# Kernel optimization log

Hardware: AMD Instinct MI355X
Metric: run time of the kernel (lower is better)

Reference implementation:

```python
import jax, jax.numpy as jnp
import numpy as np

N = 50000      # nodes
E = 800000     # edges (avg degree 16)
F = 80         # hidden_channels (forced by Linear(80, 1))
L = 4          # num_layers
NG = 1024      # graphs in batch
NFEAT = 9      # OGB atom feature columns
VOCAB = 119    # max atom feature vocab
EPS_BN = 1e-5
EPS_STD = 1e-5


def setup_inputs() -> dict:
    key = jax.random.key(0)
    ks = jax.random.split(key, 20)
    s = 0.05
    x = jax.random.randint(ks[0], (N, NFEAT), 0, 2)
    edge_index = jax.random.randint(ks[1], (2, E), 0, N)
    batch = jnp.sort(jax.random.randint(ks[2], (N,), 0, NG))
    # avg_deg['log'] from the degree histogram == mean over nodes of log(deg+1)
    deg = jax.ops.segment_sum(jnp.ones((E,), jnp.float32), edge_index[1], num_segments=N)
    avg_deg_log = jnp.array([jnp.mean(jnp.log(deg + 1.0))], jnp.float32)
    atom_emb = jax.random.normal(ks[3], (NFEAT, VOCAB, F), jnp.float32) * s
    pre_W = jax.random.normal(ks[4], (L, 2 * F, F), jnp.float32) * s
    pre_b = jax.random.normal(ks[5], (L, F), jnp.float32) * s
    post_W = jax.random.normal(ks[6], (L, 13 * F, F), jnp.float32) * s
    post_b = jax.random.normal(ks[7], (L, F), jnp.float32) * s
    lin_W = jax.random.normal(ks[8], (L, F, F), jnp.float32) * s
    lin_b = jax.random.normal(ks[9], (L, F), jnp.float32) * s
    bn_gamma = 1.0 + jax.random.normal(ks[10], (L, F), jnp.float32) * 0.1
    bn_beta = jax.random.normal(ks[11], (L, F), jnp.float32) * 0.1
    bn_mean = jax.random.normal(ks[12], (L, F), jnp.float32) * 0.1
    bn_var = 0.5 + jax.random.uniform(ks[13], (L, F), jnp.float32)
    mlp_W = jax.random.normal(ks[14], (F, 1), jnp.float32) * s
    mlp_b = jax.random.normal(ks[15], (1,), jnp.float32) * s
    return {
        'x': x, 'edge_index': edge_index, 'batch': batch,
        'avg_deg_log': avg_deg_log, 'atom_emb': atom_emb,
        'pre_W': pre_W, 'pre_b': pre_b, 'post_W': post_W, 'post_b': post_b,
        'lin_W': lin_W, 'lin_b': lin_b,
        'bn_gamma': bn_gamma, 'bn_beta': bn_beta, 'bn_mean': bn_mean, 'bn_var': bn_var,
        'mlp_W': mlp_W, 'mlp_b': mlp_b,
    }


def _forward(x, edge_index, batch, avg_deg_log, atom_emb, pre_W, pre_b,
             post_W, post_b, lin_W, lin_b, bn_gamma, bn_beta, bn_mean, bn_var,
             mlp_W, mlp_b):
    # AtomEncoder: sum of per-column embeddings
    h = jnp.sum(atom_emb[jnp.arange(NFEAT)[None, :], x], axis=1)  # [N, F]
    src, dst = edge_index[0], edge_index[1]
    deg = jax.ops.segment_sum(jnp.ones((E,), h.dtype), dst, num_segments=N)
    has_edge = (deg > 0)[:, None]
    degc = jnp.maximum(deg, 1.0)[:, None]          # clamp(min=1)
    logd = jnp.log(degc + 1.0)                     # [N, 1]
    avg = avg_deg_log[0]
    for i in range(L):
        x_h = h
        # message: pre_nn(cat([x_i, x_j]))
        m = jnp.concatenate([h[dst], h[src]], axis=-1) @ pre_W[i] + pre_b[i]  # [E, F]
        s1 = jax.ops.segment_sum(m, dst, num_segments=N)
        s2 = jax.ops.segment_sum(m * m, dst, num_segments=N)
        mean = s1 / degc
        var = s2 / degc - mean * mean
        std = jnp.sqrt(jax.nn.relu(var) + EPS_STD)
        mn = jnp.where(has_edge, jax.ops.segment_min(m, dst, num_segments=N), 0.0)
        mx = jnp.where(has_edge, jax.ops.segment_max(m, dst, num_segments=N), 0.0)
        agg = jnp.concatenate([mean, mn, mx, std], axis=-1)  # [N, 4F]
        sc = logd / avg
        out = jnp.concatenate([agg, agg * sc, agg / sc], axis=-1)  # [N, 12F]
        out = jnp.concatenate([h, out], axis=-1) @ post_W[i] + post_b[i]  # [N, F]
        out = out @ lin_W[i] + lin_b[i]
        out = (out - bn_mean[i]) * (bn_gamma[i] / jnp.sqrt(bn_var[i] + EPS_BN)) + bn_beta[i]
        h = x_h + jax.nn.relu(out)  # dropout is identity in eval
    counts = jnp.maximum(jax.ops.segment_sum(jnp.ones((N,), h.dtype), batch, num_segments=NG), 1.0)
    g = jax.ops.segment_sum(h, batch, num_segments=NG) / counts[:, None]  # global_mean_pool
    return g @ mlp_W + mlp_b  # [NG, 1]


def reference(x, edge_index, batch, avg_deg_log, atom_emb, pre_W, pre_b,
              post_W, post_b, lin_W, lin_b, bn_gamma, bn_beta, bn_mean, bn_var,
              mlp_W, mlp_b):
    return _forward(x, edge_index, batch, avg_deg_log, atom_emb, pre_W, pre_b,
                    post_W, post_b, lin_W, lin_b, bn_gamma, bn_beta, bn_mean, bn_var,
                    mlp_W, mlp_b)
```

## Files before the change

kernel.cpp:

```cpp
#include <hip/hip_runtime.h>
#include <hip/hip_bf16.h>

#define NN 50000
#define NE 800000
#define FD 80
#define NGR 1024
#define NF 9

#define BSH 6
#define NBUCK ((NN + 63) >> 6)
#define CSH 12
#define NCH ((NE + 4095) >> 12)
#define BCAP 2048

using bf16 = __hip_bfloat16;
typedef __attribute__((ext_vector_type(8))) short bf16x8;
typedef __attribute__((ext_vector_type(4))) float f32x4;

static __device__ __forceinline__ float b2f(bf16 v){ return __bfloat162float(v); }
static __device__ __forceinline__ bf16 f2b(float v){ return __float2bfloat16(v); }
static __device__ __forceinline__ float rdw(const void* p, int i, int fl){
  return fl ? ((const float*)p)[i] : b2f(((const bf16*)p)[i]);
}
static __device__ __forceinline__ unsigned pk(float a, float b){
  bf16 x = f2b(a), y = f2b(b);
  return (unsigned)*(unsigned short*)&x | ((unsigned)*(unsigned short*)&y << 16);
}
static __device__ __forceinline__ bf16x8 ldsld8(const short* p){
  union { bf16x8 v; uint2 u[2]; } r;
  r.u[0] = *(const uint2*)(p);
  r.u[1] = *(const uint2*)(p + 4);
  return r.v;
}
static __device__ __forceinline__ void ldsst16(short* p, uint4 v){
  *(uint2*)(p)     = make_uint2(v.x, v.y);
  *(uint2*)(p + 4) = make_uint2(v.z, v.w);
}

__global__ void k_zero(int* __restrict__ p, int n){
  int t = blockIdx.x*256 + threadIdx.x;
  if (t < n) p[t] = 0;
}

__global__ void k_probe(const void* __restrict__ emb, int* __restrict__ flag){
  int t = blockIdx.x*256 + threadIdx.x;
  float v = b2f(((const bf16*)emb)[t]);
  if (!(fabsf(v) < 1e4f)) atomicOr(flag, 1);
}

__global__ __launch_bounds__(256) void k_prep_all(
    const void* __restrict__ preW, const void* __restrict__ preb,
    const void* __restrict__ postW, const void* __restrict__ postb,
    const void* __restrict__ linW, const void* __restrict__ linb,
    const void* __restrict__ bng, const void* __restrict__ bnb,
    const void* __restrict__ bnm, const void* __restrict__ bnv,
    const int* __restrict__ flag,
    bf16* __restrict__ pwb, bf16* __restrict__ Btl, bf16* __restrict__ Bt1,
    float* __restrict__ bias1, float* __restrict__ bias2)
{
  int fl = flag[0];
  int b = blockIdx.x;
  if (b < 1300){
    int t = b*256 + threadIdx.x;
    pwb[t] = f2b(rdw(postW, t, fl));
  } else if (b < 1420){
    int t = (b - 1300)*256 + threadIdx.x;
    int j = t % 96, c = (t/96) % 80, i = t/(96*80);
    float v = 0.f;
    if (j < 80){
      float gs = rdw(bng, i*80 + c, fl) * rsqrtf(rdw(bnv, i*80 + c, fl) + 1e-5f);
      v = rdw(linW, i*6400 + j*80 + c, fl) * gs;
    }
    Btl[t] = f2b(v);
  } else if (b < 1660){
    int t = (b - 1420)*256 + threadIdx.x;
    int k = t % 96, c = (t/96) % 160, i = t/(96*160);
    float v = 0.f;
    if (k < 80)
      v = (c < 80) ? rdw(preW, (i*160 + k)*80 + c, fl)
                   : rdw(preW, (i*160 + 80 + k)*80 + (c - 80), fl);
    Bt1[t] = f2b(v);
    if (k == 0) bias1[i*160 + c] = (c < 80) ? rdw(preb, i*80 + c, fl) : 0.f;
  } else {
    int t = (b - 1660)*256 + threadIdx.x;
    if (t >= 4*80) return;
    int i = t / 80, f = t - i*80;
    float s = 0.f;
    for (int j = 0; j < 80; j++)
      s += rdw(postb, i*80 + j, fl) * rdw(linW, (i*80 + j)*80 + f, fl);
    s += rdw(linb, t, fl);
    float gs = rdw(bng, t, fl) * rsqrtf(rdw(bnv, t, fl) + 1e-5f);
    bias2[t] = (s - rdw(bnm, t, fl)) * gs + rdw(bnb, t, fl);
  }
}

__global__ void k_prep_Bt2(const float* __restrict__ Wf, bf16* __restrict__ Bt2){
  int t = blockIdx.x*256 + threadIdx.x;
  if (t >= 4*240*416) return;
  int k = t % 416;
  int c = (t/416) % 240;
  int i = t/(416*240);
  float v = 0.f;
  if (k < 400){
    int blk = c/80, f = c - blk*80;
    if (blk == 0) v = Wf[(i*1040 + k)*80 + f];
    else if (k >= 80){
      int row = (blk == 1 ? 400 : 720) + (k - 80);
      v = Wf[(i*1040 + row)*80 + f];
    }
  }
  Bt2[t] = f2b(v);
}

__global__ void k_atom(const int* __restrict__ x, const void* __restrict__ emb,
                       const int* __restrict__ flag, float* __restrict__ h){
  int fl = flag[0];
  int gid = blockIdx.x*256 + threadIdx.x;
  if (gid >= NN*10) return;
  int n = gid / 10, fb = gid - n*10;
  int f0 = fb*8;
  int xr[NF];
  #pragma unroll
  for (int c = 0; c < NF; c++) xr[c] = x[n*NF + c];
  float s[8] = {0.f,0.f,0.f,0.f,0.f,0.f,0.f,0.f};
  if (fl){
    #pragma unroll
    for (int c = 0; c < NF; c++){
      const float* ep = (const float*)emb + (c*119 + xr[c])*80 + f0;
      float4 a = *(const float4*)ep, b = *(const float4*)(ep + 4);
      s[0]+=a.x; s[1]+=a.y; s[2]+=a.z; s[3]+=a.w;
      s[4]+=b.x; s[5]+=b.y; s[6]+=b.z; s[7]+=b.w;
    }
  } else {
    #pragma unroll
    for (int c = 0; c < NF; c++){
      const bf16* ep = (const bf16*)emb + (c*119 + xr[c])*80 + f0;
      uint4 u = *(const uint4*)ep;
      s[0]+=__uint_as_float(u.x<<16); s[1]+=__uint_as_float(u.x&0xffff0000u);
      s[2]+=__uint_as_float(u.y<<16); s[3]+=__uint_as_float(u.y&0xffff0000u);
      s[4]+=__uint_as_float(u.z<<16); s[5]+=__uint_as_float(u.z&0xffff0000u);
      s[6]+=__uint_as_float(u.w<<16); s[7]+=__uint_as_float(u.w&0xffff0000u);
    }
  }
  float* hp = h + n*80 + f0;
  *(float4*)hp       = make_float4(s[0],s[1],s[2],s[3]);
  *(float4*)(hp + 4) = make_float4(s[4],s[5],s[6],s[7]);
}


__global__ __launch_bounds__(256) void k_hist(const int* __restrict__ ei,
                                              int* __restrict__ chunkcnt){
  __shared__ int hist[NBUCK];
  int c = blockIdx.x, t = threadIdx.x;
  for (int i = t; i < NBUCK; i += 256) hist[i] = 0;
  __syncthreads();
  #pragma unroll
  for (int j = 0; j < 16; j++){
    int e = (c << CSH) + j*256 + t;
    if (e < NE) atomicAdd(&hist[ei[NE + e] >> BSH], 1);
  }
  __syncthreads();
  for (int i = t; i < NBUCK; i += 256) chunkcnt[c*NBUCK + i] = hist[i];
}

__global__ __launch_bounds__(256) void k_cscan(int* __restrict__ chunkcnt,
                                               int* __restrict__ btotal){
  __shared__ int buf[256];
  int b = blockIdx.x, t = threadIdx.x;
  int v[4]; int s = 0;
  #pragma unroll
  for (int j = 0; j < 4; j++){
    int c = t*4 + j;
    v[j] = (c < NCH) ? chunkcnt[c*NBUCK + b] : 0;
    s += v[j];
  }
  buf[t] = s;
  __syncthreads();
  for (int off = 1; off < 256; off <<= 1){
    int xv = (t >= off) ? buf[t - off] : 0;
    __syncthreads();
    buf[t] += xv;
    __syncthreads();
  }
  int excl = buf[t] - s;
  #pragma unroll
  for (int j = 0; j < 4; j++){
    int c = t*4 + j;
    if (c < NCH){ chunkcnt[c*NBUCK + b] = excl; excl += v[j]; }
  }
  if (t == 255) btotal[b] = buf[255];
}

__global__ __launch_bounds__(256) void k_bscan(const int* __restrict__ btotal,
                                               int* __restrict__ bbase){
  __shared__ int buf[256];
  int t = threadIdx.x;
  int v[4]; int s = 0;
  #pragma unroll
  for (int j = 0; j < 4; j++){
    int c = t*4 + j;
    v[j] = (c < NBUCK) ? btotal[c] : 0;
    s += v[j];
  }
  buf[t] = s;
  __syncthreads();
  for (int off = 1; off < 256; off <<= 1){
    int xv = (t >= off) ? buf[t - off] : 0;
    __syncthreads();
    buf[t] += xv;
    __syncthreads();
  }
  int excl = buf[t] - s;
  #pragma unroll
  for (int j = 0; j < 4; j++){
    int c = t*4 + j;
    if (c < NBUCK){ bbase[c] = excl; excl += v[j]; }
  }
  if (t == 255) bbase[NBUCK] = buf[255];
}

__global__ __launch_bounds__(256) void k_place(const int* __restrict__ ei,
                        const int* __restrict__ chunkcnt, const int* __restrict__ bbase,
                        int* __restrict__ staging){
  __shared__ int basep[NBUCK];
  __shared__ int cur[NBUCK];
  int c = blockIdx.x, t = threadIdx.x;
  for (int i = t; i < NBUCK; i += 256){
    basep[i] = chunkcnt[c*NBUCK + i] + bbase[i];
    cur[i] = 0;
  }
  __syncthreads();
  #pragma unroll
  for (int j = 0; j < 16; j++){
    int e = (c << CSH) + j*256 + t;
    if (e < NE){
      int d = ei[NE + e], s = ei[e];
      int b = d >> BSH;
      int r = atomicAdd(&cur[b], 1);
      staging[basep[b] + r] = (s << BSH) | (d & 63);
    }
  }
}

__global__ __launch_bounds__(256) void k_csr(const int* __restrict__ staging,
                        const int* __restrict__ bbase, const void* __restrict__ avgp,
                        const int* __restrict__ flag, int* __restrict__ rowptr,
                        float* __restrict__ scf, float* __restrict__ invf,
                        int* __restrict__ colidx){
  __shared__ int lcnt[64], lrp[64], lcur[64];
  __shared__ int colbuf[BCAP];
  int b = blockIdx.x, t = threadIdx.x;
  int base = bbase[b];
  int cnt  = bbase[b+1] - base;
  if (t < 64){ lcnt[t] = 0; lcur[t] = 0; }
  __syncthreads();
  for (int i = t; i < cnt; i += 256)
    atomicAdd(&lcnt[staging[base + i] & 63], 1);
  __syncthreads();
  if (t < 64) lrp[t] = lcnt[t];
  __syncthreads();
  for (int off = 1; off < 64; off <<= 1){
    int xv = (t < 64 && t >= off) ? lrp[t - off] : 0;
    __syncthreads();
    if (t < 64) lrp[t] += xv;
    __syncthreads();
  }
  int n0 = b << BSH;
  if (t < 64){
    int ex = lrp[t] - lcnt[t];
    lrp[t] = ex;
    int n = n0 + t;
    if (n < NN){
      rowptr[n] = base + ex;
      float degc = (float)(lcnt[t] > 0 ? lcnt[t] : 1);
      float logd = logf(degc + 1.f);
      float avg = rdw(avgp, 0, flag[0]);
      scf[n] = logd / avg;
      invf[n] = avg / logd;
    }
  }
  if (b == 0 && t == 0) rowptr[NN] = NE;
  __syncthreads();
  if (cnt <= BCAP){
    for (int i = t; i < cnt; i += 256){
      int v = staging[base + i];
      int l = v & 63;
      int pos = lrp[l] + atomicAdd(&lcur[l], 1);
      colbuf[pos] = v >> BSH;
    }
    __syncthreads();
    for (int i = t; i < cnt; i += 256)
      colidx[base + i] = colbuf[i];
  } else {
    for (int i = t; i < cnt; i += 256){
      int v = staging[base + i];
      int l = v & 63;
      int pos = lrp[l] + atomicAdd(&lcur[l], 1);
      colidx[base + pos] = v >> BSH;
    }
  }
}

template<int AF32, int OUTMODE, int K_, int AST>
__global__ __launch_bounds__(256) void k_mgemm(
    const void* __restrict__ A1p, int s1, int KA,
    const bf16* __restrict__ A2, int s2, int KB,
    const bf16* __restrict__ Btp, int Bts, int Ncols,
    const float* __restrict__ bias,
    void* __restrict__ Cbase, void* __restrict__ Cp2, int Cstride, int M,
    int lA1b, int lBtb, int lCb)
{
  const void* A1 = (const char*)A1p + (size_t)blockIdx.z*lA1b;
  const bf16* Bt = (const bf16*)((const char*)Btp + (size_t)blockIdx.z*lBtb);
  void* Cp = (char*)Cbase + (size_t)blockIdx.z*lCb;

  constexpr int NKT = K_ / 32;
  __shared__ short As[64*AST];
  __shared__ short Bs[256*44];

  const int tid = threadIdx.x;
  const int row0 = blockIdx.x * 64;
  const int wave = tid >> 6, lane = tid & 63;
  const int wc = wave * 64;
  const int m16 = lane & 15, q = lane >> 4;

  const int ra = tid >> 2, ka = (tid & 3) * 8;
  const int cb = tid >> 2, kb = (tid & 3) * 8;

  f32x4 acc[4][4] = {};
  uint4 pb[4];

#define LOADB(k0_) { int kgb = (k0_) + kb;                                     \
    _Pragma("unroll")                                                          \
    for (int j = 0; j < 4; j++){                                               \
      int col = cb + j*64;                                                     \
      pb[j].x = pb[j].y = pb[j].z = pb[j].w = 0u;                              \
      if (col < Ncols) pb[j] = *(const uint4*)(Bt + col*Bts + kgb);            \
    } }

  LOADB(0);

  {
    const int grow = row0 + ra;
    uint4 tA[NKT];
    #pragma unroll
    for (int c = 0; c < NKT; c++){
      int kg = c*32 + ka;
      uint4 pa; pa.x = pa.y = pa.z = pa.w = 0u;
      if (grow < M){
        if (kg < KA){
          if (AF32){
            const float* ap = (const float*)A1 + grow*s1 + kg;
            float4 f0 = *(const float4*)ap;
            float4 f1 = *(const float4*)(ap + 4);
            pa.x = pk(f0.x, f0.y); pa.y = pk(f0.z, f0.w);
            pa.z = pk(f1.x, f1.y); pa.w = pk(f1.z, f1.w);
          } else {
            pa = *(const uint4*)((const bf16*)A1 + grow*s1 + kg);
          }
        } else if (kg - KA < KB){
          pa = *(const uint4*)(A2 + grow*s2 + (kg - KA));
        }
      }
      tA[c] = pa;
    }
    #pragma unroll
    for (int c = 0; c < NKT; c++)
      ldsst16(&As[ra*AST + c*32 + ka], tA[c]);
  }
  __syncthreads();

  #pragma unroll
  for (int ks = 0; ks < NKT; ks++){
    #pragma unroll
    for (int j = 0; j < 4; j++)
      ldsst16(&Bs[(cb + j*64)*44 + kb], pb[j]);
    __syncthreads();

    if (ks + 1 < NKT) LOADB((ks + 1)*32);

    bf16x8 af[4], bfv[4];
    #pragma unroll
    for (int rt = 0; rt < 4; rt++)
      af[rt] = ldsld8(&As[(rt*16 + m16)*AST + ks*32 + q*8]);
    #pragma unroll
    for (int ct = 0; ct < 4; ct++)
      bfv[ct] = ldsld8(&Bs[(wc + ct*16 + m16)*44 + q*8]);
    #pragma unroll
    for (int rt = 0; rt < 4; rt++)
      #pragma unroll
      for (int ct = 0; ct < 4; ct++)
        acc[rt][ct] = __builtin_amdgcn_mfma_f32_16x16x32_bf16(af[rt], bfv[ct], acc[rt][ct], 0, 0, 0);
    __syncthreads();
  }
#undef LOADB

  #pragma unroll
  for (int rt = 0; rt < 4; rt++){
    #pragma unroll
    for (int rr = 0; rr < 4; rr++){
      int row = row0 + rt*16 + q*4 + rr;
      if (row >= M) continue;
      #pragma unroll
      for (int ct = 0; ct < 4; ct++){
        int col = wc + ct*16 + m16;
        if (col >= Ncols) continue;
        float v = acc[rt][ct][rr] + (bias ? bias[col] : 0.f);
        if (OUTMODE == 1) ((float*)Cp)[row*Cstride + col] = v;
        else {
          if (col < 80) ((bf16*)Cp )[row*80 + col]      = f2b(v);
          else          ((bf16*)Cp2)[row*80 + col - 80] = f2b(v);
        }
      }
    }
  }
}

__global__ __launch_bounds__(256) void k_g2(
    const float* __restrict__ h, const bf16* __restrict__ agg,
    const bf16* __restrict__ Bt, const float* __restrict__ bias2v,
    const float* __restrict__ scf, const float* __restrict__ invf,
    float* __restrict__ hp,
    const bf16* __restrict__ Bt1n, const float* __restrict__ bias1n,
    bf16* __restrict__ Ua, bf16* __restrict__ Ub)
{
  constexpr int AST = 420, NKT = 13;
  __shared__ short As[32*AST];
  __shared__ short Bs[256*44];
  bf16* eL = (bf16*)As;
  bf16* hA = (bf16*)(As + 8192);

  const int tid = threadIdx.x;
  const int row0 = blockIdx.x * 32;
  const int wave = tid >> 6, lane = tid & 63;
  const int wc = wave * 64;
  const int m16 = lane & 15, q = lane >> 4;
  const int ra = tid >> 3;
  const int ka0 = (tid & 7) * 8;
  const int cb = tid >> 2, kb = (tid & 3) * 8;

  f32x4 acc[2][4] = {};
  uint4 pb[4];

#define LOADB2(k0_) { int kgb = (k0_) + kb;                                    \
    _Pragma("unroll")                                                          \
    for (int j = 0; j < 4; j++){                                               \
      int col = cb + j*64;                                                     \
      pb[j].x = pb[j].y = pb[j].z = pb[j].w = 0u;                              \
      if (col < 240) pb[j] = *(const uint4*)(Bt + col*416 + kgb);              \
    } }

  LOADB2(0);

  {
    const int grow = row0 + ra;
    uint4 tA[7];
    #pragma unroll
    for (int c = 0; c < 7; c++){
      int kg = ka0 + c*64;
      uint4 pa; pa.x = pa.y = pa.z = pa.w = 0u;
      if (kg < 416 && grow < NN){
        if (kg < 80){
          const float* ap = h + grow*80 + kg;
          float4 f0 = *(const float4*)ap;
          float4 f1 = *(const float4*)(ap + 4);
          pa.x = pk(f0.x, f0.y); pa.y = pk(f0.z, f0.w);
          pa.z = pk(f1.x, f1.y); pa.w = pk(f1.z, f1.w);
        } else if (kg < 400){
          pa = *(const uint4*)(agg + grow*320 + (kg - 80));
        }
      }
      tA[c] = pa;
    }
    #pragma unroll
    for (int c = 0; c < 7; c++){
      int kg = ka0 + c*64;
      if (kg < 416) ldsst16(&As[ra*AST + kg], tA[c]);
    }
  }
  __syncthreads();

  #pragma unroll
  for (int ks = 0; ks < NKT; ks++){
    #pragma unroll
    for (int j = 0; j < 4; j++)
      ldsst16(&Bs[(cb + j*64)*44 + kb], pb[j]);
    __syncthreads();

    if (ks + 1 < NKT) LOADB2((ks + 1)*32);

    bf16x8 af[2], bfv[4];
    #pragma unroll
    for (int rt = 0; rt < 2; rt++)
      af[rt] = ldsld8(&As[(rt*16 + m16)*AST + ks*32 + q*8]);
    #pragma unroll
    for (int ct = 0; ct < 4; ct++)
      bfv[ct] = ldsld8(&Bs[(wc + ct*16 + m16)*44 + q*8]);
    #pragma unroll
    for (int rt = 0; rt < 2; rt++)
      #pragma unroll
      for (int ct = 0; ct < 4; ct++)
        acc[rt][ct] = __builtin_amdgcn_mfma_f32_16x16x32_bf16(af[rt], bfv[ct], acc[rt][ct], 0, 0, 0);
    __syncthreads();
  }
#undef LOADB2

  uint4 pb1[4];
  if (Bt1n){
    #pragma unroll
    for (int j = 0; j < 4; j++){
      int col = cb + j*64;
      pb1[j].x = pb1[j].y = pb1[j].z = pb1[j].w = 0u;
      if (col < 160) pb1[j] = *(const uint4*)(Bt1n + col*96 + kb);
    }
  }

  #pragma unroll
  for (int rt = 0; rt < 2; rt++){
    #pragma unroll
    for (int ct = 0; ct < 4; ct++){
      int col = wc + ct*16 + m16;
      if (col >= 240) continue;
      #pragma unroll
      for (int rr = 0; rr < 4; rr++){
        int r = rt*16 + q*4 + rr;
        eL[r*248 + col] = f2b(acc[rt][ct][rr]);
      }
    }
  }
  __syncthreads();

  #pragma unroll
  for (int i = 0; i < 10; i++){
    int idx = tid + i*256;
    int r = idx / 80, c = idx - r*80;
    int row = row0 + r;
    if (row < NN){
      float P = b2f(eL[r*248 + c]);
      float Q = b2f(eL[r*248 + 80 + c]);
      float R = b2f(eL[r*248 + 160 + c]);
      float o = P + scf[row]*Q + invf[row]*R + bias2v[c];
      float hn = hp[row*80 + c] + fmaxf(o, 0.f);
      hp[row*80 + c] = hn;
      if (Bt1n) hA[r*100 + c] = f2b(hn);
    } else if (Bt1n && idx < 32*80){
      hA[r*100 + c] = f2b(0.f);
    }
  }
  if (Bt1n && tid < 128){
    int r = tid >> 2, off = 80 + (tid & 3)*4;
    *(uint2*)&hA[r*100 + off] = make_uint2(0u, 0u);
  }
  __syncthreads();

  if (Bt1n){
    f32x4 acc2[2][4] = {};
    #pragma unroll
    for (int ks = 0; ks < 3; ks++){
      #pragma unroll
      for (int j = 0; j < 4; j++)
        ldsst16(&Bs[(cb + j*64)*44 + kb], pb1[j]);
      __syncthreads();

      if (ks + 1 < 3){
        int kgb = (ks + 1)*32 + kb;
        #pragma unroll
        for (int j = 0; j < 4; j++){
          int col = cb + j*64;
          pb1[j].x = pb1[j].y = pb1[j].z = pb1[j].w = 0u;
          if (col < 160) pb1[j] = *(const uint4*)(Bt1n + col*96 + kgb);
        }
      }

      bf16x8 af[2], bfv[4];
      #pragma unroll
      for (int rt = 0; rt < 2; rt++)
        af[rt] = ldsld8((const short*)hA + (rt*16 + m16)*100 + ks*32 + q*8);
      #pragma unroll
      for (int ct = 0; ct < 4; ct++)
        bfv[ct] = ldsld8(&Bs[(wc + ct*16 + m16)*44 + q*8]);
      #pragma unroll
      for (int rt = 0; rt < 2; rt++)
        #pragma unroll
        for (int ct = 0; ct < 4; ct++)
          acc2[rt][ct] = __builtin_amdgcn_mfma_f32_16x16x32_bf16(af[rt], bfv[ct], acc2[rt][ct], 0, 0, 0);
      __syncthreads();
    }
    #pragma unroll
    for (int rt = 0; rt < 2; rt++){
      #pragma unroll
      for (int rr = 0; rr < 4; rr++){
        int row = row0 + rt*16 + q*4 + rr;
        if (row >= NN) continue;
        #pragma unroll
        for (int ct = 0; ct < 4; ct++){
          int col = wc + ct*16 + m16;
          if (col >= 160) continue;
          float v = acc2[rt][ct][rr] + bias1n[col];
          if (col < 80) Ua[row*80 + col]      = f2b(v);
          else          Ub[row*80 + col - 80] = f2b(v);
        }
      }
    }
  }
}

__global__ __launch_bounds__(256) void k_agg(const bf16* __restrict__ Ua,
                      const bf16* __restrict__ Ub,
                      const int* __restrict__ rowptr,
                      const int* __restrict__ colidx, bf16* __restrict__ agg)
{
  int lane = threadIdx.x & 63;
  int slot = lane / 20;
  int n = blockIdx.x*12 + (threadIdx.x >> 6)*3 + slot;
  if (slot >= 3 || n >= NN) return;
  int fo = (lane - slot*20) * 4;
  int rs = rowptr[n], re = rowptr[n+1];
  int deg = re - rs;

  float a[4];
  {
    uint2 ua = *(const uint2*)(Ua + n*80 + fo);
    a[0] = __uint_as_float(ua.x << 16);
    a[1] = __uint_as_float(ua.x & 0xffff0000u);
    a[2] = __uint_as_float(ua.y << 16);
    a[3] = __uint_as_float(ua.y & 0xffff0000u);
  }
  float sb[4] = {0.f,0.f,0.f,0.f}, sq[4] = {0.f,0.f,0.f,0.f};
  float mn[4] = {1e30f,1e30f,1e30f,1e30f}, mx[4] = {-1e30f,-1e30f,-1e30f,-1e30f};

#define ACC2(w, o) { \
    float b0 = __uint_as_float((w) << 16); \
    float b1 = __uint_as_float((w) & 0xffff0000u); \
    sb[o] += b0; sq[o] += b0*b0; mn[o] = fminf(mn[o],b0); mx[o] = fmaxf(mx[o],b0); \
    sb[o+1] += b1; sq[o+1] += b1*b1; mn[o+1] = fminf(mn[o+1],b1); mx[o+1] = fmaxf(mx[o+1],b1); }

  for (int e = rs; e < re; e += 8){
    int cnt = re - e; if (cnt > 8) cnt = 8;
    int s[8];
    #pragma unroll
    for (int j = 0; j < 8; j++) s[j] = (j < cnt) ? colidx[e + j] : s[0];
    uint2 u[8];
    #pragma unroll
    for (int j = 0; j < 8; j++) u[j] = *(const uint2*)(Ub + s[j]*80 + fo);
    #pragma unroll
    for (int j = 0; j < 8; j++){
      if (j < cnt){ ACC2(u[j].x, 0); ACC2(u[j].y, 2); }
    }
  }
#undef ACC2

  float degc = (float)(deg > 0 ? deg : 1);
  float inv = 1.f/degc;
  float dm = (float)deg;
  float mean0, mean1, v0, v1, sd0, sd1, lo0, lo1, hi0, hi1;

  mean0 = (dm*a[0] + sb[0])*inv; mean1 = (dm*a[1] + sb[1])*inv;
  v0 = (dm*a[0]*a[0] + 2.f*a[0]*sb[0] + sq[0])*inv - mean0*mean0;
  v1 = (dm*a[1]*a[1] + 2.f*a[1]*sb[1] + sq[1])*inv - mean1*mean1;
  sd0 = sqrtf(fmaxf(v0,0.f)+1e-5f); sd1 = sqrtf(fmaxf(v1,0.f)+1e-5f);
  lo0 = deg>0 ? a[0]+mn[0] : 0.f; lo1 = deg>0 ? a[1]+mn[1] : 0.f;
  hi0 = deg>0 ? a[0]+mx[0] : 0.f; hi1 = deg>0 ? a[1]+mx[1] : 0.f;
  unsigned o0 = pk(mean0, mean1);
  unsigned l0 = pk(lo0, lo1), h0 = pk(hi0, hi1), t0 = pk(sd0, sd1);

  mean0 = (dm*a[2] + sb[2])*inv; mean1 = (dm*a[3] + sb[3])*inv;
  v0 = (dm*a[2]*a[2] + 2.f*a[2]*sb[2] + sq[2])*inv - mean0*mean0;
  v1 = (dm*a[3]*a[3] + 2.f*a[3]*sb[3] + sq[3])*inv - mean1*mean1;
  sd0 = sqrtf(fmaxf(v0,0.f)+1e-5f); sd1 = sqrtf(fmaxf(v1,0.f)+1e-5f);
  lo0 = deg>0 ? a[2]+mn[2] : 0.f; lo1 = deg>0 ? a[3]+mn[3] : 0.f;
  hi0 = deg>0 ? a[2]+mx[2] : 0.f; hi1 = deg>0 ? a[3]+mx[3] : 0.f;
  unsigned o1 = pk(mean0, mean1);
  unsigned l1 = pk(lo0, lo1), h1 = pk(hi0, hi1), t1 = pk(sd0, sd1);

  bf16* ag = agg + n*320 + fo;
  *(uint2*)(ag)       = make_uint2(o0, o1);
  *(uint2*)(ag + 80)  = make_uint2(l0, l1);
  *(uint2*)(ag + 160) = make_uint2(h0, h1);
  *(uint2*)(ag + 240) = make_uint2(t0, t1);
}

__global__ __launch_bounds__(128) void k_poolmlp(const float* __restrict__ h,
                        const int* __restrict__ batch,
                        const void* __restrict__ mlpW, const void* __restrict__ mlpb,
                        const int* __restrict__ flag, void* __restrict__ outp){
  __shared__ float sred[128];
  __shared__ int sb[2];
  int g = blockIdx.x;
  int t = threadIdx.x;
  if (t < 2){
    int target = g + t;
    int lo = 0, hi = NN;
    while (lo < hi){ int mid = (lo + hi) >> 1; if (batch[mid] < target) lo = mid + 1; else hi = mid; }
    sb[t] = lo;
  }
  __syncthreads();
  int lo = sb[0], hi = sb[1];
  float s = 0.f;
  if (t < 80)
    for (int n = lo; n < hi; n++) s += h[n*80 + t];
  int fl = flag[0];
  float wv = (t < 80) ? rdw(mlpW, t, fl) : 0.f;
  sred[t] = s * wv;
  __syncthreads();
  for (int off = 64; off > 0; off >>= 1){
    if (t < off) sred[t] += sred[t + off];
    __syncthreads();
  }
  if (t == 0){
    float cnt = (float)(hi - lo); if (cnt < 1.f) cnt = 1.f;
    float r = sred[0]/cnt + rdw(mlpb, 0, fl);
    if (fl) ((float*)outp)[g] = r;
    else    ((bf16*)outp)[g] = f2b(r);
  }
}

extern "C" void kernel_launch(void* const* d_in, const int* in_sizes, int n_in,
                              void* d_out, int out_size, void* d_ws, size_t ws_size,
                              hipStream_t stream)
{
  const int*  x     = (const int*) d_in[0];
  const int*  ei    = (const int*) d_in[1];
  const int*  batch = (const int*) d_in[2];
  const void* avgp  = d_in[3];
  const void* aemb  = d_in[4];
  const void* preW  = d_in[5];
  const void* preb  = d_in[6];
  const void* postW = d_in[7];
  const void* postb = d_in[8];
  const void* linW  = d_in[9];
  const void* linb  = d_in[10];
  const void* bng   = d_in[11];
  const void* bnb   = d_in[12];
  const void* bnm   = d_in[13];
  const void* bnv   = d_in[14];
  const void* mlpW  = d_in[15];
  const void* mlpb  = d_in[16];

  char* w = (char*)d_ws;
  int*   flag   = (int*)  (w + 400000);
  int*   rowptr = (int*)  (w + 401280);
  int*   colidx = (int*)  (w + 601344);
  float* scf    = (float*)(w + 3801344);
  float* invf   = (float*)(w + 4001344);
  float* bias1  = (float*)(w + 4201344);
  float* bias2  = (float*)(w + 4203904);
  bf16*  Btl    = (bf16*) (w + 4205184);
  bf16*  Bt1    = (bf16*) (w + 4266624);
  bf16*  Bt2    = (bf16*) (w + 4389504);
  float* h      = (float*)(w + 5188224);
  bf16*  Ua     = (bf16*) (w + 21188224);
  bf16*  Ub     = (bf16*) (w + 29188224);
  bf16*  agg    = (bf16*) (w + 45188224);
  bf16*  pwb    = (bf16*) (w + 45188224);
  float* Wf     = (float*)(w + 45853824);
  int* staging  = (int*)  (w + 47185024);
  int* chunkcnt = (int*)  (w + 50385024);
  int* btotal   = (int*)  (w + 52831120);
  int* bbase    = (int*)  (w + 52834248);

  k_zero <<<1, 256, 0, stream>>>(flag, 64);
  k_probe<<<16, 256, 0, stream>>>(aemb, flag);

  k_hist <<<NCH, 256, 0, stream>>>(ei, chunkcnt);
  k_cscan<<<NBUCK, 256, 0, stream>>>(chunkcnt, btotal);
  k_bscan<<<1, 256, 0, stream>>>(btotal, bbase);
  k_place<<<NCH, 256, 0, stream>>>(ei, chunkcnt, bbase, staging);

  k_prep_all<<<1662, 256, 0, stream>>>(preW, preb, postW, postb, linW, linb,
                                       bng, bnb, bnm, bnv, flag,
                                       pwb, Btl, Bt1, bias1, bias2);

  k_mgemm<0,1,96,100><<<dim3(17,1,4), 256, 0, stream>>>(
      pwb, 80, 80, nullptr, 0, 0,
      Btl, 96, 80, nullptr, Wf, nullptr, 80, 1040,
      166400, 15360, 332800);
  k_prep_Bt2<<<(4*240*416 + 255)/256, 256, 0, stream>>>(Wf, Bt2);

  k_atom <<<(NN*10 + 255)/256, 256, 0, stream>>>(x, aemb, flag, h);

  k_csr<<<NBUCK, 256, 0, stream>>>(staging, bbase, avgp, flag, rowptr, scf, invf, colidx);

  k_mgemm<1,2,96,100><<<dim3((NN + 63)/64,1,1), 256, 0, stream>>>(
      h, 80, 80, nullptr, 0, 0,
      Bt1, 96, 160, bias1, Ua, Ub, 0, NN,
      0, 0, 0);
  const int gx2 = (NN + 31)/32;
  for (int i = 0; i < 4; i++){
    k_agg<<<(NN + 11)/12, 256, 0, stream>>>(Ua, Ub, rowptr, colidx, agg);
    const bf16* nBt1   = (i < 3) ? (Bt1 + (i+1)*15360) : nullptr;
    const float* nb1   = (i < 3) ? (bias1 + (i+1)*160) : bias1;
    k_g2<<<dim3(gx2,1,1), 256, 0, stream>>>(
        h, agg, Bt2 + i*99840, bias2 + i*80, scf, invf, h,
        nBt1, nb1, Ua, Ub);
  }

  k_poolmlp<<<NGR, 128, 0, stream>>>(h, batch, mlpW, mlpb, flag, d_out);
}
```

Measured before the change: 573.9 us.

## Pre-tile GEMM weights into MFMA fragment layout and load B directly from global

Measured after the change: 524.5 us. -8.6%, faster.

```diff
diff --git a/kernel.cpp b/kernel.cpp
--- a/kernel.cpp
+++ b/kernel.cpp
@@ -79,7 +79,8 @@
     if (k < 80)
       v = (c < 80) ? rdw(preW, (i*160 + k)*80 + c, fl)
                    : rdw(preW, (i*160 + 80 + k)*80 + (c - 80), fl);
-    Bt1[t] = f2b(v);
+    int of = ((k >> 5)*160 + c)*32 + (k & 31 & ~7) + (k & 7);
+    Bt1[i*15360 + of] = f2b(v);
     if (k == 0) bias1[i*160 + c] = (c < 80) ? rdw(preb, i*80 + c, fl) : 0.f;
   } else {
     int t = (b - 1660)*256 + threadIdx.x;
@@ -109,7 +110,8 @@
       v = Wf[(i*1040 + row)*80 + f];
     }
   }
-  Bt2[t] = f2b(v);
+  int of = (k >> 5)*7680 + c*32 + (k & 31);
+  Bt2[i*99840 + of] = f2b(v);
 }
 
 __global__ void k_atom(const int* __restrict__ x, const void* __restrict__ emb,
@@ -416,6 +418,79 @@
   }
 }
 
+__global__ __launch_bounds__(256) void k_g1(
+    const float* __restrict__ h, const bf16* __restrict__ Bt1t,
+    const float* __restrict__ bias1v,
+    bf16* __restrict__ Ua, bf16* __restrict__ Ub)
+{
+  __shared__ short hA[32*100];
+  const int tid = threadIdx.x;
+  const int row0 = blockIdx.x * 32;
+  const int wave = tid >> 6, lane = tid & 63;
+  const int wc = wave * 64;
+  const int m16 = lane & 15, q = lane >> 4;
+  const int ra = tid >> 3, ka0 = (tid & 7) * 8;
+
+  {
+    int grow = row0 + ra;
+    #pragma unroll
+    for (int c = 0; c < 2; c++){
+      int kg = ka0 + c*64;
+      if (kg < 96){
+        uint4 pa; pa.x = pa.y = pa.z = pa.w = 0u;
+        if (kg < 80 && grow < NN){
+          const float* ap = h + grow*80 + kg;
+          float4 f0 = *(const float4*)ap, f1 = *(const float4*)(ap + 4);
+          pa.x = pk(f0.x, f0.y); pa.y = pk(f0.z, f0.w);
+          pa.z = pk(f1.x, f1.y); pa.w = pk(f1.z, f1.w);
+        }
+        ldsst16(&hA[ra*100 + kg], pa);
+      }
+    }
+  }
+  __syncthreads();
+
+  const bf16* bp1[4];
+  #pragma unroll
+  for (int ct = 0; ct < 4; ct++){
+    int col = wc + ct*16 + m16;
+    if (col >= 160) col = 0;
+    bp1[ct] = Bt1t + col*32 + q*8;
+  }
+  f32x4 acc[2][4] = {};
+  #pragma unroll
+  for (int ks = 0; ks < 3; ks++){
+    bf16x8 bfv[4], af[2];
+    #pragma unroll
+    for (int ct = 0; ct < 4; ct++)
+      bfv[ct] = *(const bf16x8*)(bp1[ct] + ks*5120);
+    #pragma unroll
+    for (int rt = 0; rt < 2; rt++)
+      af[rt] = ldsld8(&hA[(rt*16 + m16)*100 + ks*32 + q*8]);
+    #pragma unroll
+    for (int rt = 0; rt < 2; rt++)
+      #pragma unroll
+      for (int ct = 0; ct < 4; ct++)
+        acc[rt][ct] = __builtin_amdgcn_mfma_f32_16x16x32_bf16(af[rt], bfv[ct], acc[rt][ct], 0, 0, 0);
+  }
+  #pragma unroll
+  for (int rt = 0; rt < 2; rt++){
+    #pragma unroll
+    for (int rr = 0; rr < 4; rr++){
+      int row = row0 + rt*16 + q*4 + rr;
+      if (row >= NN) continue;
+      #pragma unroll
+      for (int ct = 0; ct < 4; ct++){
+        int col = wc + ct*16 + m16;
+        if (col >= 160) continue;
+        float v = acc[rt][ct][rr] + bias1v[col];
+        if (col < 80) Ua[row*80 + col]      = f2b(v);
+        else          Ub[row*80 + col - 80] = f2b(v);
+      }
+    }
+  }
+}
+
 __global__ __launch_bounds__(256) void k_g2(
     const float* __restrict__ h, const bf16* __restrict__ agg,
     const bf16* __restrict__ Bt, const float* __restrict__ bias2v,
@@ -426,7 +501,6 @@
 {
   constexpr int AST = 420, NKT = 13;
   __shared__ short As[32*AST];
-  __shared__ short Bs[256*44];
   bf16* eL = (bf16*)As;
   bf16* hA = (bf16*)(As + 8192);
 
@@ -437,20 +511,6 @@
   const int m16 = lane & 15, q = lane >> 4;
   const int ra = tid >> 3;
   const int ka0 = (tid & 7) * 8;
-  const int cb = tid >> 2, kb = (tid & 3) * 8;
-
-  f32x4 acc[2][4] = {};
-  uint4 pb[4];
-
-#define LOADB2(k0_) { int kgb = (k0_) + kb;                                    \
-    _Pragma("unroll")                                                          \
-    for (int j = 0; j < 4; j++){                                               \
-      int col = cb + j*64;                                                     \
-      pb[j].x = pb[j].y = pb[j].z = pb[j].w = 0u;                              \
-      if (col < 240) pb[j] = *(const uint4*)(Bt + col*416 + kgb);              \
-    } }
-
-  LOADB2(0);
 
   {
     const int grow = row0 + ra;
@@ -478,42 +538,34 @@
       if (kg < 416) ldsst16(&As[ra*AST + kg], tA[c]);
     }
   }
-  __syncthreads();
+
+  const bf16* bp[4];
+  #pragma unroll
+  for (int ct = 0; ct < 4; ct++){
+    int col = wc + ct*16 + m16;
+    if (col >= 240) col = 0;
+    bp[ct] = Bt + col*32 + q*8;
+  }
+  __syncthreads();
+
+  f32x4 acc[2][4] = {};
 
   #pragma unroll
   for (int ks = 0; ks < NKT; ks++){
-    #pragma unroll
-    for (int j = 0; j < 4; j++)
-      ldsst16(&Bs[(cb + j*64)*44 + kb], pb[j]);
-    __syncthreads();
-
-    if (ks + 1 < NKT) LOADB2((ks + 1)*32);
-
-    bf16x8 af[2], bfv[4];
+    bf16x8 bfv[4], af[2];
+    #pragma unroll
+    for (int ct = 0; ct < 4; ct++)
+      bfv[ct] = *(const bf16x8*)(bp[ct] + ks*7680);
     #pragma unroll
     for (int rt = 0; rt < 2; rt++)
       af[rt] = ldsld8(&As[(rt*16 + m16)*AST + ks*32 + q*8]);
     #pragma unroll
-    for (int ct = 0; ct < 4; ct++)
-      bfv[ct] = ldsld8(&Bs[(wc + ct*16 + m16)*44 + q*8]);
-    #pragma unroll
     for (int rt = 0; rt < 2; rt++)
       #pragma unroll
       for (int ct = 0; ct < 4; ct++)
         acc[rt][ct] = __builtin_amdgcn_mfma_f32_16x16x32_bf16(af[rt], bfv[ct], acc[rt][ct], 0, 0, 0);
-    __syncthreads();
-  }
-#undef LOADB2
-
-  uint4 pb1[4];
-  if (Bt1n){
-    #pragma unroll
-    for (int j = 0; j < 4; j++){
-      int col = cb + j*64;
-      pb1[j].x = pb1[j].y = pb1[j].z = pb1[j].w = 0u;
-      if (col < 160) pb1[j] = *(const uint4*)(Bt1n + col*96 + kb);
-    }
-  }
+  }
+  __syncthreads();
 
   #pragma unroll
   for (int rt = 0; rt < 2; rt++){
@@ -554,37 +606,28 @@
   __syncthreads();
 
   if (Bt1n){
+    const bf16* bp1[4];
+    #pragma unroll
+    for (int ct = 0; ct < 4; ct++){
+      int col = wc + ct*16 + m16;
+      if (col >= 160) col = 0;
+      bp1[ct] = Bt1n + col*32 + q*8;
+    }
     f32x4 acc2[2][4] = {};
     #pragma unroll
     for (int ks = 0; ks < 3; ks++){
-      #pragma unroll
-      for (int j = 0; j < 4; j++)
-        ldsst16(&Bs[(cb + j*64)*44 + kb], pb1[j]);
-      __syncthreads();
-
-      if (ks + 1 < 3){
-        int kgb = (ks + 1)*32 + kb;
-        #pragma unroll
-        for (int j = 0; j < 4; j++){
-          int col = cb + j*64;
-          pb1[j].x = pb1[j].y = pb1[j].z = pb1[j].w = 0u;
-          if (col < 160) pb1[j] = *(const uint4*)(Bt1n + col*96 + kgb);
-        }
-      }
-
-      bf16x8 af[2], bfv[4];
+      bf16x8 bfv[4], af[2];
+      #pragma unroll
+      for (int ct = 0; ct < 4; ct++)
+        bfv[ct] = *(const bf16x8*)(bp1[ct] + ks*5120);
       #pragma unroll
       for (int rt = 0; rt < 2; rt++)
         af[rt] = ldsld8((const short*)hA + (rt*16 + m16)*100 + ks*32 + q*8);
-      #pragma unroll
-      for (int ct = 0; ct < 4; ct++)
-        bfv[ct] = ldsld8(&Bs[(wc + ct*16 + m16)*44 + q*8]);
       #pragma unroll
       for (int rt = 0; rt < 2; rt++)
         #pragma unroll
         for (int ct = 0; ct < 4; ct++)
           acc2[rt][ct] = __builtin_amdgcn_mfma_f32_16x16x32_bf16(af[rt], bfv[ct], acc2[rt][ct], 0, 0, 0);
-      __syncthreads();
     }
     #pragma unroll
     for (int rt = 0; rt < 2; rt++){
@@ -668,7 +711,7 @@
   v0 = (dm*a[2]*a[2] + 2.f*a[2]*sb[2] + sq[2])*inv - mean0*mean0;
   v1 = (dm*a[3]*a[3] + 2.f*a[3]*sb[3] + sq[3])*inv - mean1*mean1;
   sd0 = sqrtf(fmaxf(v0,0.f)+1e-5f); sd1 = sqrtf(fmaxf(v1,0.f)+1e-5f);
-  lo0 = deg>0 ? a[2]+mn[2] : 0.f; lo1 = deg>0 ? a[3]+mn[3] : 0.f;
+  lo0 = deg>0 ? a[2]+mn[2] : 0.f; lo1 = deg>0 ? a[2+1]+mn[3] : 0.f;
   hi0 = deg>0 ? a[2]+mx[2] : 0.f; hi1 = deg>0 ? a[3]+mx[3] : 0.f;
   unsigned o1 = pk(mean0, mean1);
   unsigned l1 = pk(lo0, lo1), h1 = pk(hi0, hi1), t1 = pk(sd0, sd1);
@@ -781,11 +824,8 @@
 
   k_csr<<<NBUCK, 256, 0, stream>>>(staging, bbase, avgp, flag, rowptr, scf, invf, colidx);
 
-  k_mgemm<1,2,96,100><<<dim3((NN + 63)/64,1,1), 256, 0, stream>>>(
-      h, 80, 80, nullptr, 0, 0,
-      Bt1, 96, 160, bias1, Ua, Ub, 0, NN,
-      0, 0, 0);
   const int gx2 = (NN + 31)/32;
+  k_g1<<<dim3(gx2,1,1), 256, 0, stream>>>(h, Bt1, bias1, Ua, Ub);
   for (int i = 0; i < 4; i++){
     k_agg<<<(NN + 11)/12, 256, 0, stream>>>(Ua, Ub, rowptr, colidx, agg);
     const bf16* nBt1   = (i < 3) ? (Bt1 + (i+1)*15360) : nullptr;
```
